# Performance work log

Measured on AMD Instinct MI355X. Metric: run time of the kernel, lower is better.

## Reference

```python
import jax, jax.numpy as jnp
import numpy as np

NVAR, B, C, H, W = 3, 4, 256, 64, 64
C1 = C // 2          # dat channels (nc)
C2 = C - C1
HEADS = 4
HC = C1 // HEADS     # head channels
STRIDE = 4
KS = 4
HK, WK = H // STRIDE, W // STRIDE
NS = HK * WK         # n_sample
RPE_H, RPE_W = 2 * H - 1, 2 * W - 1
NPAIR = 3


def _grid_sample(img, grid):
    # img [B,C,Hi,Wi]; grid [B,Hg,Wg,2] = (x,y) in [-1,1]; bilinear, align_corners=True, zero-pad
    Bn, Cn, Hi, Wi = img.shape
    x = (grid[..., 0] + 1.0) * 0.5 * (Wi - 1)
    y = (grid[..., 1] + 1.0) * 0.5 * (Hi - 1)
    x0 = jnp.floor(x)
    y0 = jnp.floor(y)
    wx = x - x0
    wy = y - y0
    x0i = x0.astype(jnp.int32)
    y0i = y0.astype(jnp.int32)
    imt = img.transpose(0, 2, 3, 1)  # [B,Hi,Wi,C]
    bidx = jnp.arange(Bn)[:, None, None]

    def corner(yi, xi, wgt):
        ok = ((xi >= 0) & (xi < Wi) & (yi >= 0) & (yi < Hi)).astype(img.dtype)
        val = imt[bidx, jnp.clip(yi, 0, Hi - 1), jnp.clip(xi, 0, Wi - 1)]  # [B,Hg,Wg,C]
        return val * (wgt * ok)[..., None]

    out = (corner(y0i, x0i, (1 - wx) * (1 - wy))
           + corner(y0i, x0i + 1, wx * (1 - wy))
           + corner(y0i + 1, x0i, (1 - wx) * wy)
           + corner(y0i + 1, x0i + 1, wx * wy))
    return out.transpose(0, 3, 1, 2)  # [B,C,Hg,Wg]


def _ref_points(hk, wk):
    # normalized sampling-grid reference points, (y,x) order
    ry = (jnp.linspace(0.5, hk - 0.5, hk) / (hk - 1.0)) * 2.0 - 1.0
    rx = (jnp.linspace(0.5, wk - 0.5, wk) / (wk - 1.0)) * 2.0 - 1.0
    return jnp.stack(jnp.meshgrid(ry, rx, indexing='ij'), axis=-1)  # [hk,wk,2]


def _q_grid(h, w):
    gy = (jnp.arange(h, dtype=jnp.float32) / (h - 1.0)) * 2.0 - 1.0
    gx = (jnp.arange(w, dtype=jnp.float32) / (w - 1.0)) * 2.0 - 1.0
    return jnp.stack(jnp.meshgrid(gy, gx, indexing='ij'), axis=-1).reshape(h * w, 2)


def _conv1x1(x, w, b=None):
    y = jnp.einsum('oc,bchw->bohw', w, x)
    return y if b is None else y + b[None, :, None, None]


def _dat_block(q_in, kv_in, pWq, pbq, pWk, pbk, pWv, pbv, pWo, pbo,
               pdw_w, pdw_b, pln_g, pln_b, ppw_w, prpe):
    Bn = q_in.shape[0]
    q = _conv1x1(q_in, pWq, pbq)  # [B,C1,H,W]
    # offset net: depthwise 4x4 stride-4 conv -> channel LN -> GELU -> 1x1 conv to 2
    off = jax.lax.conv_general_dilated(
        q, pdw_w, (STRIDE, STRIDE), 'VALID',
        dimension_numbers=('NCHW', 'OIHW', 'NCHW'),
        feature_group_count=C1) + pdw_b[None, :, None, None]  # [B,C1,HK,WK]
    mu = off.mean(axis=1, keepdims=True)
    var = ((off - mu) ** 2).mean(axis=1, keepdims=True)
    off = (off - mu) * jax.lax.rsqrt(var + 1e-5) * pln_g[None, :, None, None] + pln_b[None, :, None, None]
    off = jax.nn.gelu(off, approximate=False)
    offset = _conv1x1(off, ppw_w).transpose(0, 2, 3, 1)  # [B,HK,WK,2] (dy,dx)
    # offset_range_factor = -1 -> no tanh scaling, clamp pos into [-1,1]
    pos = jnp.clip(offset + _ref_points(HK, WK)[None], -1.0, 1.0)  # [B,HK,WK,2]
    xs = _grid_sample(kv_in, pos[..., ::-1])  # sample kv at deformed points -> [B,C1,HK,WK]
    k = _conv1x1(xs, pWk, pbk).reshape(Bn, HEADS, HC, NS)
    v = _conv1x1(xs, pWv, pbv).reshape(Bn, HEADS, HC, NS)
    qh = q.reshape(Bn, HEADS, HC, H * W)
    attn = jnp.einsum('bhcm,bhcn->bhmn', qh, k) * (HC ** -0.5)  # [B,h,HW,NS]
    # relative position bias sampled from rpe table
    disp = (_q_grid(H, W)[None, :, None, :] - pos.reshape(Bn, 1, NS, 2)) * 0.5  # [B,HW,NS,2]
    rpe_b = jnp.broadcast_to(prpe[None], (Bn, HEADS, RPE_H, RPE_W))
    bias = _grid_sample(rpe_b, disp[..., ::-1])  # [B,h,HW,NS]
    attn = jax.nn.softmax(attn + bias, axis=-1)
    out = jnp.einsum('bhmn,bhcn->bhcm', attn, v).reshape(Bn, C1, H, W)
    return _conv1x1(out, pWo, pbo)


def _forward(xs, params):
    results = []
    num = 0
    for i in range(NVAR):
        res = xs[i]
        for j in range(i):
            attn_out = _dat_block(xs[i][:, :C1], xs[j][:, :C1],
                                  *(p[num] for p in params))
            # torch: res -= -cat(zeros[:,:C2], attn)  => add attn on channels C2:
            res = res.at[:, C2:].add(attn_out)
            num += 1
        results.append(res)
    return jnp.stack(results)  # [NVAR,B,C,H,W]


def setup_inputs() -> dict:
    key = jax.random.key(0)
    ks = jax.random.split(key, 4)
    d = {}
    for n, k in zip(['x0', 'x1', 'x2'], jax.random.split(ks[0], 3)):
        d[n] = jax.random.normal(k, (B, C, H, W), jnp.float32)

    def w(k, shape, s=0.02):
        return jax.random.normal(k, shape, jnp.float32) * s

    kk = jax.random.split(ks[1], 8)
    d['Wq'] = w(kk[0], (NPAIR, C1, C1))
    d['bq'] = jnp.zeros((NPAIR, C1), jnp.float32)
    d['Wk'] = w(kk[1], (NPAIR, C1, C1))
    d['bk'] = jnp.zeros((NPAIR, C1), jnp.float32)
    d['Wv'] = w(kk[2], (NPAIR, C1, C1))
    d['bv'] = jnp.zeros((NPAIR, C1), jnp.float32)
    d['Wo'] = w(kk[3], (NPAIR, C1, C1))
    d['bo'] = jnp.zeros((NPAIR, C1), jnp.float32)
    d['dw_w'] = w(kk[4], (NPAIR, C1, 1, KS, KS), 0.1)
    d['dw_b'] = jnp.zeros((NPAIR, C1), jnp.float32)
    d['ln_g'] = jnp.ones((NPAIR, C1), jnp.float32)
    d['ln_b'] = jnp.zeros((NPAIR, C1), jnp.float32)
    d['pw_w'] = w(kk[5], (NPAIR, 2, C1), 0.1)
    d['rpe'] = w(kk[6], (NPAIR, HEADS, RPE_H, RPE_W), 0.01)
    return d


def reference(x0, x1, x2, Wq, bq, Wk, bk, Wv, bv, Wo, bo,
              dw_w, dw_b, ln_g, ln_b, pw_w, rpe):
    params = (Wq, bq, Wk, bk, Wv, bv, Wo, bo, dw_w, dw_b, ln_g, ln_b, pw_w, rpe)
    out = _forward([x0, x1, x2], params)
    flow = jnp.zeros((NVAR, x0.shape[0]), out.dtype)
    return out, flow
```

## Files before the change

### kernel.cpp

```cpp
#include <hip/hip_runtime.h>
#include <math.h>

#define NVAR 3
#define BB 4
#define CC 256
#define C1 128
#define HEADS 4
#define HH 64
#define WW 64
#define HW 4096
#define RPE_W 127
#define NP 3
#define SCALE 0.17677669529663687f

typedef short bf16x8 __attribute__((ext_vector_type(8)));
typedef float f32x4 __attribute__((ext_vector_type(4)));
typedef __bf16 bf16x2 __attribute__((ext_vector_type(2)));

__device__ __forceinline__ unsigned short f2bf(float f) {
    unsigned int u = __float_as_uint(f);
    u += 0x7fffu + ((u >> 16) & 1u);
    return (unsigned short)(u >> 16);
}
__device__ __forceinline__ float bflo(unsigned u) { return __uint_as_float(u << 16); }
__device__ __forceinline__ float bfhi(unsigned u) { return __uint_as_float(u & 0xffff0000u); }

__device__ __forceinline__ float dot2bf(unsigned a, unsigned b, float c) {
#if __has_builtin(__builtin_amdgcn_fdot2_f32_bf16)
    return __builtin_amdgcn_fdot2_f32_bf16(__builtin_bit_cast(bf16x2, a),
                                           __builtin_bit_cast(bf16x2, b), c, false);
#else
    return c + bflo(a) * bflo(b) + bfhi(a) * bfhi(b);
#endif
}

__global__ __launch_bounds__(256) void prep_copy(const float* __restrict__ rpe,
                                                 const float* __restrict__ Wq,
                                                 const float* __restrict__ Wo,
                                                 const float* __restrict__ Wk,
                                                 const float* __restrict__ Wv,
                                                 const float* __restrict__ x0,
                                                 unsigned short* __restrict__ tabbf,
                                                 unsigned short* __restrict__ wqh,
                                                 unsigned short* __restrict__ woh,
                                                 unsigned short* __restrict__ wkh,
                                                 unsigned short* __restrict__ wvh,
                                                 float* __restrict__ out) {
    int blk = blockIdx.x;
    if (blk >= 24) {
        const long long n4 = (long long)BB * CC * HW / 4;
        long long i = (long long)(blk - 24) * 256 + threadIdx.x;
        const long long stride = 1024LL * 256;
        for (; i < n4 + 12; i += stride) {
            if (i < n4) ((float4*)out)[i] = ((const float4*)x0)[i];
            else out[3LL * BB * CC * HW + (i - n4)] = 0.f;
        }
        return;
    }
    if (blk < 12) {
        const float* src = rpe + (long long)blk * RPE_W * RPE_W;
        unsigned short* dst = tabbf + (long long)blk * 16384;
        for (int idx = threadIdx.x; idx < 16384; idx += 256) {
            int y = idx >> 7, x = idx & 127;
            float v = (y < RPE_W && x < RPE_W) ? src[y * RPE_W + x] : 0.f;
            dst[idx] = f2bf(v);
        }
    } else if (blk < 15) {
        int p = blk - 12;
        for (int i = threadIdx.x; i < 16384; i += 256)
            wqh[p * 16384 + i] = f2bf(Wq[p * 16384 + i]);
    } else if (blk < 18) {
        int p = blk - 15;
        for (int i = threadIdx.x; i < 16384; i += 256)
            woh[p * 16384 + i] = f2bf(Wo[p * 16384 + i]);
    } else if (blk < 21) {
        int p = blk - 18;
        for (int i = threadIdx.x; i < 16384; i += 256)
            wkh[p * 16384 + i] = f2bf(Wk[p * 16384 + i]);
    } else {
        int p = blk - 21;
        for (int i = threadIdx.x; i < 16384; i += 256)
            wvh[p * 16384 + i] = f2bf(Wv[p * 16384 + i]);
    }
}

__global__ __launch_bounds__(256) void conv_q(const float* __restrict__ x1,
                                              const float* __restrict__ x2,
                                              const unsigned short* __restrict__ wqh,
                                              const float* __restrict__ bq,
                                              unsigned short* __restrict__ qbf,
                                              float* __restrict__ out) {
    __shared__ unsigned short qlds[4][16][136];
    int wid = threadIdx.x >> 6, lane = threadIdx.x & 63;
    int g = lane >> 4, lm = lane & 15;
    int gw = blockIdx.x * 4 + wid;
    int mt = gw & 255;
    int pbi = gw >> 8;
    int merged = pbi >> 2;
    int b = pbi & 3;
    const float* X = (merged ? x2 : x1) + (long long)b * CC * HW;
    int m = mt * 16 + lm;
    int qi = merged + 1;
    float* outc = out + (((long long)(qi * 4 + b)) * CC) * HW + m;

    bf16x8 bh[4];
#pragma unroll
    for (int ksl = 0; ksl < 4; ksl++) {
        float v[8];
#pragma unroll
        for (int j = 0; j < 8; j++) {
            int k = ksl * 32 + 8 * g + j;
            v[j] = X[(long long)k * HW + m];
            outc[(long long)k * HW] = v[j];
        }
        union { unsigned u[4]; bf16x8 v; } H;
#pragma unroll
        for (int t = 0; t < 4; t++)
            H.u[t] = (unsigned)f2bf(v[2 * t]) | ((unsigned)f2bf(v[2 * t + 1]) << 16);
        bh[ksl] = H.v;
    }

    f32x4 zero = {0.f, 0.f, 0.f, 0.f};
    unsigned short* ql = &qlds[wid][lm][0];
    int qq = lane >> 4, cg = lane & 15;

    for (int rep = 0; rep <= merged; rep++) {
        int p = merged ? (1 + rep) : 0;
        int pb = p * 4 + b;
        const unsigned short* WH = wqh + p * 16384;
#pragma unroll
        for (int ct2 = 0; ct2 < 4; ct2++) {
            int ct0 = 2 * ct2, ct1 = ct0 + 1;
            f32x4 a0 = zero, a1 = zero;
#pragma unroll
            for (int ksl = 0; ksl < 4; ksl++) {
                bf16x8 Ah0 = *(const bf16x8*)(WH + (ct0 * 16 + lm) * 128 + ksl * 32 + 8 * g);
                bf16x8 Ah1 = *(const bf16x8*)(WH + (ct1 * 16 + lm) * 128 + ksl * 32 + 8 * g);
                a0 = __builtin_amdgcn_mfma_f32_16x16x32_bf16(Ah0, bh[ksl], a0, 0, 0, 0);
                a1 = __builtin_amdgcn_mfma_f32_16x16x32_bf16(Ah1, bh[ksl], a1, 0, 0, 0);
            }
            float q0[4], q1[4];
#pragma unroll
            for (int r = 0; r < 4; r++) {
                q0[r] = a0[r] + bq[p * 128 + ct0 * 16 + 4 * g + r];
                q1[r] = a1[r] + bq[p * 128 + ct1 * 16 + 4 * g + r];
            }
            *(unsigned*)(ql + ct0 * 16 + 4 * g) =
                (unsigned)f2bf(q0[0] * SCALE) | ((unsigned)f2bf(q0[1] * SCALE) << 16);
            *(unsigned*)(ql + ct0 * 16 + 4 * g + 2) =
                (unsigned)f2bf(q0[2] * SCALE) | ((unsigned)f2bf(q0[3] * SCALE) << 16);
            *(unsigned*)(ql + ct1 * 16 + 4 * g) =
                (unsigned)f2bf(q1[0] * SCALE) | ((unsigned)f2bf(q1[1] * SCALE) << 16);
            *(unsigned*)(ql + ct1 * 16 + 4 * g + 2) =
                (unsigned)f2bf(q1[2] * SCALE) | ((unsigned)f2bf(q1[3] * SCALE) << 16);
        }
        unsigned short* Yb = qbf + ((long long)pb * HW + mt * 16) * 128;
#pragma unroll
        for (int i = 0; i < 4; i++) {
            int row = i * 4 + qq;
            uint4 vv = *(const uint4*)&qlds[wid][row][cg * 8];
            *(uint4*)(Yb + row * 128 + cg * 8) = vv;
        }
    }
}

__global__ __launch_bounds__(256) void mid_kernel(const unsigned short* __restrict__ qbf,
                                                  const float* __restrict__ dw_w,
                                                  const float* __restrict__ dw_b,
                                                  const float* __restrict__ ln_g,
                                                  const float* __restrict__ ln_b,
                                                  const float* __restrict__ pw_w,
                                                  const float* __restrict__ x0,
                                                  const float* __restrict__ x1,
                                                  float* __restrict__ posb,
                                                  uint4* __restrict__ prmb,
                                                  unsigned short* __restrict__ xT) {
    __shared__ char sm[40960];
    int blk = blockIdx.x;
    int tid = threadIdx.x;
    if (blk < 192) {
        unsigned short* qs = (unsigned short*)sm;
        float (*dwout)[128] = (float(*)[128])(sm + 32768);
        int pb = blk >> 4, hk = blk & 15;
        int p = pb >> 2;
        int c = tid & 127;
        int wk0 = tid >> 7;
        const float* dwp_g = dw_w + (p * 128 + c) * 16;
        float dwp[16];
#pragma unroll
        for (int j = 0; j < 16; j++) dwp[j] = dwp_g[j] * (1.f / SCALE);
        float acc[8];
#pragma unroll
        for (int o = 0; o < 8; o++) acc[o] = dw_b[p * 128 + c];
        const unsigned short* Q = qbf + ((long long)pb * HW + hk * 256) * 128;
        for (int pass = 0; pass < 2; pass++) {
            __syncthreads();
#pragma unroll
            for (int it = 0; it < 8; it++) {
                int idx = tid + it * 256;
                int mloc = idx >> 4, cg = idx & 15;
                *(uint4*)(qs + mloc * 128 + cg * 8) =
                    *(const uint4*)(Q + (long long)(pass * 128 + mloc) * 128 + cg * 8);
            }
            __syncthreads();
#pragma unroll
            for (int o = 0; o < 8; o++) {
                int wk = wk0 + o * 2;
                float a = acc[o];
#pragma unroll
                for (int kyl = 0; kyl < 2; kyl++)
#pragma unroll
                    for (int kx = 0; kx < 4; kx++)
                        a += bflo((unsigned)qs[(kyl * 64 + wk * 4 + kx) * 128 + c])
                             * dwp[(pass * 2 + kyl) * 4 + kx];
                acc[o] = a;
            }
        }
        __syncthreads();
#pragma unroll
        for (int o = 0; o < 8; o++) dwout[wk0 + o * 2][c] = acc[o];
        __syncthreads();
        int wid = tid >> 6, lane = tid & 63;
        for (int i = 0; i < 4; i++) {
            int wk = wid * 4 + i;
            int s = hk * 16 + wk;
            float a0 = dwout[wk][lane], a1 = dwout[wk][lane + 64];
            float s1 = a0 + a1;
#pragma unroll
            for (int o = 1; o < 64; o <<= 1) s1 += __shfl_xor(s1, o);
            float mu = s1 * (1.f / 128.f);
            float d0 = a0 - mu, d1 = a1 - mu;
            float v2 = d0 * d0 + d1 * d1;
#pragma unroll
            for (int o = 1; o < 64; o <<= 1) v2 += __shfl_xor(v2, o);
            float rs = rsqrtf(v2 * (1.f / 128.f) + 1e-5f);
            int c0 = lane, c1 = lane + 64;
            float y0 = d0 * rs * ln_g[p * 128 + c0] + ln_b[p * 128 + c0];
            float y1 = d1 * rs * ln_g[p * 128 + c1] + ln_b[p * 128 + c1];
            float g0 = 0.5f * y0 * (1.f + erff(y0 * 0.70710678118654752f));
            float g1 = 0.5f * y1 * (1.f + erff(y1 * 0.70710678118654752f));
            float o0 = pw_w[(p * 2 + 0) * 128 + c0] * g0
                     + pw_w[(p * 2 + 0) * 128 + c1] * g1;
            float o1 = pw_w[(p * 2 + 1) * 128 + c0] * g0
                     + pw_w[(p * 2 + 1) * 128 + c1] * g1;
#pragma unroll
            for (int o = 1; o < 64; o <<= 1) o0 += __shfl_xor(o0, o);
#pragma unroll
            for (int o = 1; o < 64; o <<= 1) o1 += __shfl_xor(o1, o);
            if (lane == 0) {
                int wk2 = s & 15;
                float refy = (hk + 0.5f) * (2.f / 15.f) - 1.f;
                float refx = (wk2 + 0.5f) * (2.f / 15.f) - 1.f;
                float py = fminf(fmaxf(o0 + refy, -1.f), 1.f);
                float px = fminf(fmaxf(o1 + refx, -1.f), 1.f);
                int pbn = pb * 256 + s;
                posb[pbn * 2 + 0] = py;
                posb[pbn * 2 + 1] = px;
                float cy = 31.5f * (1.f - py), cx = 31.5f * (1.f - px);
                float yf = floorf(cy), xf = floorf(cx);
                float wy = cy - yf, wx = cx - xf;
                int Y0 = (int)yf, X0 = (int)xf;
                uint4 v;
                v.x = (unsigned)f2bf((1.f - wy) * (1.f - wx))
                    | ((unsigned)f2bf((1.f - wy) * wx) << 16);
                v.y = (unsigned)f2bf(wy * (1.f - wx))
                    | ((unsigned)f2bf(wy * wx) << 16);
                v.z = (unsigned)((Y0 * 128 + X0) * 2);
                v.w = 0;
                prmb[pbn] = v;
            }
        }
    } else {
        float (*ld2)[65] = (float(*)[65])sm;
        int rem = blk - 192;
        int v = rem >> 10;
        int rem1 = rem & 1023;
        int b = rem1 >> 8;
        int rem2 = rem1 & 255;
        int ct = rem2 >> 6;
        int mt = rem2 & 63;
        const float* src = ((v == 0) ? x0 : x1) + (long long)b * CC * HW
                           + (long long)(ct * 32) * HW + mt * 64;
#pragma unroll
        for (int it = 0; it < 2; it++) {
            int c = tid >> 3, x4 = (tid & 7) + it * 8;
            float4 w = *(const float4*)(src + (long long)c * HW + x4 * 4);
            ld2[c][x4 * 4 + 0] = w.x;
            ld2[c][x4 * 4 + 1] = w.y;
            ld2[c][x4 * 4 + 2] = w.z;
            ld2[c][x4 * 4 + 3] = w.w;
        }
        __syncthreads();
        int m = tid >> 2, cg = tid & 3;
        union { unsigned u[4]; } pk;
#pragma unroll
        for (int t = 0; t < 4; t++) {
            unsigned short h0 = f2bf(ld2[cg * 8 + 2 * t][m]);
            unsigned short h1 = f2bf(ld2[cg * 8 + 2 * t + 1][m]);
            pk.u[t] = (unsigned)h0 | ((unsigned)h1 << 16);
        }
        *(uint4*)(xT + (((long long)(v * 4 + b)) * HW + mt * 64 + m) * 128
                  + ct * 32 + cg * 8) = *(uint4*)pk.u;
    }
}

__global__ __launch_bounds__(256) void sample_kv(const unsigned short* __restrict__ xT,
                                                 const float* __restrict__ posb,
                                                 const unsigned short* __restrict__ wkh,
                                                 const unsigned short* __restrict__ wvh,
                                                 const float* __restrict__ bk,
                                                 const float* __restrict__ bv,
                                                 unsigned short* __restrict__ kbf,
                                                 unsigned short* __restrict__ vbf) {
    __shared__ unsigned short xls[32 * 128];
    int blk = blockIdx.x;
    int pb = blk >> 3;
    int nt = blk & 7;
    int p = pb >> 2, b = pb & 3;
    int n0 = nt * 32;
    int tid = threadIdx.x;

    {
        int nl = tid >> 3, co = tid & 7;
        int n = n0 + nl;
        float py = posb[(pb * 256 + n) * 2 + 0];
        float px = posb[(pb * 256 + n) * 2 + 1];
        float yi = (py + 1.f) * 31.5f, xi = (px + 1.f) * 31.5f;
        yi = fminf(fmaxf(yi, 0.f), 63.f);
        xi = fminf(fmaxf(xi, 0.f), 63.f);
        int y0 = min((int)yi, 62);
        int x0i = min((int)xi, 62);
        float wy = yi - (float)y0, wx = xi - (float)x0i;
        float w00 = (1.f - wy) * (1.f - wx), w01 = (1.f - wy) * wx;
        float w10 = wy * (1.f - wx), w11 = wy * wx;
        int vsel = (p == 2) ? 1 : 0;
        const unsigned short* base = xT + ((long long)(vsel * 4 + b)) * HW * 128;
        int m00 = y0 * 64 + x0i;
        char* dst = (char*)xls;
#pragma unroll
        for (int cb = 0; cb < 2; cb++) {
            int c0 = co * 16 + cb * 8;
            bf16x8 a = *(const bf16x8*)(base + (long long)m00 * 128 + c0);
            bf16x8 bb = *(const bf16x8*)(base + (long long)(m00 + 1) * 128 + c0);
            bf16x8 cc = *(const bf16x8*)(base + (long long)(m00 + 64) * 128 + c0);
            bf16x8 dd = *(const bf16x8*)(base + (long long)(m00 + 65) * 128 + c0);
            union { unsigned u[4]; bf16x8 v; } R;
#pragma unroll
            for (int t = 0; t < 4; t++) {
                float r0 = w00 * bflo((unsigned)(unsigned short)a[2 * t])
                         + w01 * bflo((unsigned)(unsigned short)bb[2 * t])
                         + w10 * bflo((unsigned)(unsigned short)cc[2 * t])
                         + w11 * bflo((unsigned)(unsigned short)dd[2 * t]);
                float r1 = w00 * bflo((unsigned)(unsigned short)a[2 * t + 1])
                         + w01 * bflo((unsigned)(unsigned short)bb[2 * t + 1])
                         + w10 * bflo((unsigned)(unsigned short)cc[2 * t + 1])
                         + w11 * bflo((unsigned)(unsigned short)dd[2 * t + 1]);
                R.u[t] = (unsigned)f2bf(r0) | ((unsigned)f2bf(r1) << 16);
            }
            *(bf16x8*)(dst + ((nl * 256 + c0 * 2) ^ ((nl & 7) << 4))) = R.v;
        }
    }
    __syncthreads();

    int wid = tid >> 6, lane = tid & 63;
    int g = lane >> 4, lm = lane & 15;
    int ntile = wid & 1, isv = wid >> 1;
    int nl = ntile * 16 + lm;
    const char* srcl = (const char*)xls;
    bf16x8 xf[4];
#pragma unroll
    for (int ks = 0; ks < 4; ks++)
        xf[ks] = *(const bf16x8*)(srcl + ((nl * 256 + (ks * 32 + 8 * g) * 2)
                                          ^ ((nl & 7) << 4)));
    f32x4 zero = {0.f, 0.f, 0.f, 0.f};
    if (!isv) {
        const unsigned short* WK = wkh + p * 16384;
#pragma unroll
        for (int ct = 0; ct < 8; ct++) {
            f32x4 acc = zero;
#pragma unroll
            for (int ks = 0; ks < 4; ks++) {
                bf16x8 wf = *(const bf16x8*)(WK + (ct * 16 + lm) * 128 + ks * 32 + 8 * g);
                acc = __builtin_amdgcn_mfma_f32_16x16x32_bf16(xf[ks], wf, acc, 0, 0, 0);
            }
            float bias = bk[p * 128 + ct * 16 + lm];
#pragma unroll
            for (int r = 0; r < 4; r++) {
                int n = n0 + ntile * 16 + 4 * g + r;
                kbf[((long long)pb * 256 + n) * 128 + ct * 16 + lm] = f2bf(acc[r] + bias);
            }
        }
    } else {
        const unsigned short* WV = wvh + p * 16384;
#pragma unroll
        for (int ct = 0; ct < 8; ct++) {
            f32x4 acc = zero;
#pragma unroll
            for (int ks = 0; ks < 4; ks++) {
                bf16x8 wf = *(const bf16x8*)(WV + (ct * 16 + lm) * 128 + ks * 32 + 8 * g);
                acc = __builtin_amdgcn_mfma_f32_16x16x32_bf16(wf, xf[ks], acc, 0, 0, 0);
            }
#pragma unroll
            for (int r = 0; r < 4; r++) {
                int c = ct * 16 + 4 * g + r;
                vbf[((long long)pb * 128 + c) * 256 + n0 + ntile * 16 + lm]
                    = f2bf(acc[r] + bv[p * 128 + c]);
            }
        }
    }
}

__global__ __launch_bounds__(256, 4) void attn_mfma(
        const unsigned short* __restrict__ qbf,
        const unsigned short* __restrict__ kbf,
        const unsigned short* __restrict__ vbf,
        const unsigned short* __restrict__ tabbf,
        const uint4* __restrict__ prmb,
        unsigned short* __restrict__ obf) {
    __shared__ unsigned short tab[16384 + 8];
    __shared__ uint4 prm[256];
    int tid = threadIdx.x;
    int wid = tid >> 6, lane = tid & 63;
    int g = lane >> 4, lm = lane & 15;
    int bid = blockIdx.x;
    int my = bid & 63;
    int h = (bid >> 6) & 3;
    int b = (bid >> 8) & 3;
    int p = bid >> 10;
    int pb = p * 4 + b;

    {
        const uint4* ts = (const uint4*)(tabbf + (long long)(p * 4 + h) * 16384);
        uint4* td = (uint4*)tab;
#pragma unroll
        for (int i = 0; i < 8; i++) td[tid + i * 256] = ts[tid + i * 256];
        prm[tid] = prmb[pb * 256 + tid];
    }
    __syncthreads();

    int mx = (wid << 4) + lm;

    bf16x8 qf = *(const bf16x8*)(qbf + ((long long)pb * HW + my * 64 + mx) * 128
                                 + h * 32 + 8 * g);
    const unsigned short* kbase = kbf + ((long long)pb * 256 + lm) * 128
                                  + h * 32 + 8 * g;
    f32x4 zero = {0.f, 0.f, 0.f, 0.f};
    f32x4 acc[16];
    __builtin_amdgcn_s_setprio(1);
#pragma unroll
    for (int ni = 0; ni < 16; ni++) {
        bf16x8 kf = *(const bf16x8*)(kbase + ni * 16 * 128);
        acc[ni] = __builtin_amdgcn_mfma_f32_16x16x32_bf16(kf, qf, zero, 0, 0, 0);
    }
    __builtin_amdgcn_s_setprio(0);

    int laneoff = (my * 128 + mx) * 2;
    const char* tb = (const char*)tab;
#pragma unroll
    for (int ni = 0; ni < 16; ni++) {
#pragma unroll
        for (int r = 0; r < 4; r++) {
            int n = ni * 16 + 4 * g + r;
            uint4 pw = prm[n];
            int va = (int)pw.z + laneoff;
            int va4 = va & ~3;
            int sh = va & 3;
            unsigned r0 = *(const unsigned*)(tb + va4);
            unsigned r1 = *(const unsigned*)(tb + va4 + 4);
            unsigned r2 = *(const unsigned*)(tb + va4 + 256);
            unsigned r3 = *(const unsigned*)(tb + va4 + 260);
            unsigned p0 = __builtin_amdgcn_alignbyte(r1, r0, sh);
            unsigned p1 = __builtin_amdgcn_alignbyte(r3, r2, sh);
            float t = acc[ni][r];
            t = dot2bf(p0, pw.x, t);
            t = dot2bf(p1, pw.y, t);
            acc[ni][r] = t;
        }
    }

    float mxv = -1e30f;
#pragma unroll
    for (int ni = 0; ni < 16; ni++)
        mxv = fmaxf(mxv, fmaxf(fmaxf(acc[ni][0], acc[ni][1]),
                               fmaxf(acc[ni][2], acc[ni][3])));
    mxv = fmaxf(mxv, __shfl_xor(mxv, 16));
    mxv = fmaxf(mxv, __shfl_xor(mxv, 32));
    float sum = 0.f;
    unsigned dwA[16], dwB[16];
#pragma unroll
    for (int ni = 0; ni < 16; ni++) {
        float e0 = __expf(acc[ni][0] - mxv);
        float e1 = __expf(acc[ni][1] - mxv);
        float e2 = __expf(acc[ni][2] - mxv);
        float e3 = __expf(acc[ni][3] - mxv);
        sum += (e0 + e1) + (e2 + e3);
        asm("v_cvt_pk_bf16_f32 %0, %1, %2" : "=v"(dwA[ni]) : "v"(e0), "v"(e1));
        asm("v_cvt_pk_bf16_f32 %0, %1, %2" : "=v"(dwB[ni]) : "v"(e2), "v"(e3));
    }
    sum += __shfl_xor(sum, 16);
    sum += __shfl_xor(sum, 32);

    int src0 = ((g & 1) << 5) + lm;
    int src1 = src0 + 16;
    bool sel = (g >> 1) != 0;
    const unsigned short* vb0 = vbf + ((long long)pb * 128 + h * 32 + lm) * 256
                                + 8 * g;
    f32x4 o0 = zero, o1 = zero;
#pragma unroll
    for (int st = 0; st < 8; st++) {
        unsigned d0a = __shfl(dwA[2 * st], src0), d0b = __shfl(dwA[2 * st + 1], src0);
        unsigned d1a = __shfl(dwB[2 * st], src0), d1b = __shfl(dwB[2 * st + 1], src0);
        unsigned d2a = __shfl(dwA[2 * st], src1), d2b = __shfl(dwA[2 * st + 1], src1);
        unsigned d3a = __shfl(dwB[2 * st], src1), d3b = __shfl(dwB[2 * st + 1], src1);
        union { unsigned u[4]; bf16x8 v; } pf;
        pf.u[0] = sel ? d0b : d0a;
        pf.u[1] = sel ? d1b : d1a;
        pf.u[2] = sel ? d2b : d2a;
        pf.u[3] = sel ? d3b : d3a;
        bf16x8 v0 = *(const bf16x8*)(vb0 + st * 32);
        bf16x8 v1 = *(const bf16x8*)(vb0 + 4096 + st * 32);
        __builtin_amdgcn_s_setprio(1);
        o0 = __builtin_amdgcn_mfma_f32_16x16x32_bf16(v0, pf.v, o0, 0, 0, 0);
        o1 = __builtin_amdgcn_mfma_f32_16x16x32_bf16(v1, pf.v, o1, 0, 0, 0);
        __builtin_amdgcn_s_setprio(0);
    }

    float inv = 1.f / sum;
    __syncthreads();
    {
        unsigned short* rw = tab + wid * 640 + lm * 40;
        *(unsigned*)(rw + g * 4) =
            (unsigned)f2bf(o0[0] * inv) | ((unsigned)f2bf(o0[1] * inv) << 16);
        *(unsigned*)(rw + g * 4 + 2) =
            (unsigned)f2bf(o0[2] * inv) | ((unsigned)f2bf(o0[3] * inv) << 16);
        *(unsigned*)(rw + 16 + g * 4) =
            (unsigned)f2bf(o1[0] * inv) | ((unsigned)f2bf(o1[1] * inv) << 16);
        *(unsigned*)(rw + 16 + g * 4 + 2) =
            (unsigned)f2bf(o1[2] * inv) | ((unsigned)f2bf(o1[3] * inv) << 16);
    }
    int row = lane >> 2, cb = lane & 3;
    uint4 vv = *(const uint4*)(tab + wid * 640 + row * 40 + cb * 8);
    *(uint4*)(obf + ((long long)pb * HW + my * 64 + wid * 16 + row) * 128
              + h * 32 + cb * 8) = vv;
}

__global__ __launch_bounds__(256) void conv_wo(const float* __restrict__ x1,
                                               const float* __restrict__ x2,
                                               const unsigned short* __restrict__ obf,
                                               const unsigned short* __restrict__ woh,
                                               const float* __restrict__ bo,
                                               float* __restrict__ out) {
    int wid = threadIdx.x >> 6, lane = threadIdx.x & 63;
    int g = lane >> 4, lm = lane & 15;
    int gw = blockIdx.x * 4 + wid;
    int mt = gw & 255;
    int b = (gw >> 8) & 3;
    int vs = gw >> 10;
    int m = mt * 16 + lm;
    int np = vs + 1;

    f32x4 acc[8];
#pragma unroll
    for (int ct = 0; ct < 8; ct++) acc[ct] = (f32x4){0.f, 0.f, 0.f, 0.f};

    for (int pi = 0; pi < np; pi++) {
        int p = vs ? (1 + pi) : 0;
        const unsigned short* Om = obf + ((long long)(p * 4 + b) * HW + m) * 128;
        const unsigned short* WH = woh + p * 16384;
#pragma unroll
        for (int ksl = 0; ksl < 4; ksl++) {
            bf16x8 bh = *(const bf16x8*)(Om + ksl * 32 + 8 * g);
#pragma unroll
            for (int ct = 0; ct < 8; ct++) {
                bf16x8 A = *(const bf16x8*)(WH + (ct * 16 + lm) * 128 + ksl * 32 + 8 * g);
                acc[ct] = __builtin_amdgcn_mfma_f32_16x16x32_bf16(A, bh, acc[ct], 0, 0, 0);
            }
        }
    }

    int qi = vs + 1;
    const float* xq = (vs ? x2 : x1) + (long long)b * CC * HW;
#pragma unroll
    for (int ct = 0; ct < 8; ct++)
#pragma unroll
        for (int r = 0; r < 4; r++) {
            int c = ct * 16 + 4 * g + r;
            float bias = vs ? (bo[128 + c] + bo[256 + c]) : bo[c];
            float base = xq[(long long)(128 + c) * HW + m];
            out[(((long long)(qi * 4 + b)) * CC + 128 + c) * HW + m]
                = base + acc[ct][r] + bias;
        }
}

extern "C" void kernel_launch(void* const* d_in, const int* in_sizes, int n_in,
                              void* d_out, int out_size, void* d_ws, size_t ws_size,
                              hipStream_t stream) {
    const float* x0 = (const float*)d_in[0];
    const float* x1 = (const float*)d_in[1];
    const float* x2 = (const float*)d_in[2];
    const float* Wq = (const float*)d_in[3];
    const float* bq = (const float*)d_in[4];
    const float* Wk = (const float*)d_in[5];
    const float* bk = (const float*)d_in[6];
    const float* Wv = (const float*)d_in[7];
    const float* bv = (const float*)d_in[8];
    const float* Wo = (const float*)d_in[9];
    const float* bo = (const float*)d_in[10];
    const float* dw_w = (const float*)d_in[11];
    const float* dw_b = (const float*)d_in[12];
    const float* ln_g = (const float*)d_in[13];
    const float* ln_b = (const float*)d_in[14];
    const float* pw_w = (const float*)d_in[15];
    const float* rpe = (const float*)d_in[16];
    float* out = (float*)d_out;

    float* ws = (float*)d_ws;
    unsigned short* obf = (unsigned short*)ws;
    float* posb = ws + 6291456;
    unsigned short* xT = (unsigned short*)(posb + 6144);
    unsigned short* qbf = xT + 4194304;
    unsigned short* kbf = qbf + 12582912;
    unsigned short* vbf = kbf + 393216;
    unsigned short* tabbf = vbf + 393216;
    uint4* prmb = (uint4*)(tabbf + 196608);
    unsigned short* wqh = (unsigned short*)(prmb + 3072);
    unsigned short* woh = wqh + 49152;
    unsigned short* wkh = woh + 49152;
    unsigned short* wvh = wkh + 49152;

    prep_copy<<<1048, 256, 0, stream>>>(rpe, Wq, Wo, Wk, Wv, x0, tabbf,
                                        wqh, woh, wkh, wvh, out);
    conv_q<<<512, 256, 0, stream>>>(x1, x2, wqh, bq, qbf, out);
    mid_kernel<<<2240, 256, 0, stream>>>(qbf, dw_w, dw_b, ln_g, ln_b, pw_w,
                                         x0, x1, posb, prmb, xT);
    sample_kv<<<96, 256, 0, stream>>>(xT, posb, wkh, wvh, bk, bv, kbf, vbf);
    attn_mfma<<<3072, 256, 0, stream>>>(qbf, kbf, vbf, tabbf, prmb, obf);
    conv_wo<<<512, 256, 0, stream>>>(x1, x2, obf, woh, bo, out);
}
```

Measured before the change: 163.1 us.

## Split attention key dimension across two wave groups with LDS softmax merge

```diff
diff --git a/kernel.cpp b/kernel.cpp
--- a/kernel.cpp
+++ b/kernel.cpp
@@ -410,7 +410,7 @@
     }
 }
 
-__global__ __launch_bounds__(256, 4) void attn_mfma(
+__global__ __launch_bounds__(512, 4) void attn_mfma(
         const unsigned short* __restrict__ qbf,
         const unsigned short* __restrict__ kbf,
         const unsigned short* __restrict__ vbf,
@@ -422,6 +422,8 @@
     int tid = threadIdx.x;
     int wid = tid >> 6, lane = tid & 63;
     int g = lane >> 4, lm = lane & 15;
+    int nh = wid >> 2;
+    int mq = wid & 3;
     int bid = blockIdx.x;
     int my = bid & 63;
     int h = (bid >> 6) & 3;
@@ -433,23 +435,24 @@
         const uint4* ts = (const uint4*)(tabbf + (long long)(p * 4 + h) * 16384);
         uint4* td = (uint4*)tab;
 #pragma unroll
-        for (int i = 0; i < 8; i++) td[tid + i * 256] = ts[tid + i * 256];
-        prm[tid] = prmb[pb * 256 + tid];
+        for (int i = 0; i < 4; i++) td[tid + i * 512] = ts[tid + i * 512];
+        if (tid < 256) prm[tid] = prmb[pb * 256 + tid];
     }
     __syncthreads();
 
-    int mx = (wid << 4) + lm;
+    int mx = (mq << 4) + lm;
+    int nb = nh * 128;
 
     bf16x8 qf = *(const bf16x8*)(qbf + ((long long)pb * HW + my * 64 + mx) * 128
                                  + h * 32 + 8 * g);
     const unsigned short* kbase = kbf + ((long long)pb * 256 + lm) * 128
                                   + h * 32 + 8 * g;
     f32x4 zero = {0.f, 0.f, 0.f, 0.f};
-    f32x4 acc[16];
+    f32x4 acc[8];
     __builtin_amdgcn_s_setprio(1);
 #pragma unroll
-    for (int ni = 0; ni < 16; ni++) {
-        bf16x8 kf = *(const bf16x8*)(kbase + ni * 16 * 128);
+    for (int ni = 0; ni < 8; ni++) {
+        bf16x8 kf = *(const bf16x8*)(kbase + (nb + ni * 16) * 128);
         acc[ni] = __builtin_amdgcn_mfma_f32_16x16x32_bf16(kf, qf, zero, 0, 0, 0);
     }
     __builtin_amdgcn_s_setprio(0);
@@ -457,10 +460,10 @@
     int laneoff = (my * 128 + mx) * 2;
     const char* tb = (const char*)tab;
 #pragma unroll
-    for (int ni = 0; ni < 16; ni++) {
+    for (int ni = 0; ni < 8; ni++) {
 #pragma unroll
         for (int r = 0; r < 4; r++) {
-            int n = ni * 16 + 4 * g + r;
+            int n = nb + ni * 16 + 4 * g + r;
             uint4 pw = prm[n];
             int va = (int)pw.z + laneoff;
             int va4 = va & ~3;
@@ -478,36 +481,46 @@
         }
     }
 
-    float mxv = -1e30f;
-#pragma unroll
-    for (int ni = 0; ni < 16; ni++)
-        mxv = fmaxf(mxv, fmaxf(fmaxf(acc[ni][0], acc[ni][1]),
-                               fmaxf(acc[ni][2], acc[ni][3])));
-    mxv = fmaxf(mxv, __shfl_xor(mxv, 16));
-    mxv = fmaxf(mxv, __shfl_xor(mxv, 32));
-    float sum = 0.f;
-    unsigned dwA[16], dwB[16];
-#pragma unroll
-    for (int ni = 0; ni < 16; ni++) {
-        float e0 = __expf(acc[ni][0] - mxv);
-        float e1 = __expf(acc[ni][1] - mxv);
-        float e2 = __expf(acc[ni][2] - mxv);
-        float e3 = __expf(acc[ni][3] - mxv);
-        sum += (e0 + e1) + (e2 + e3);
+    float mloc = -1e30f;
+#pragma unroll
+    for (int ni = 0; ni < 8; ni++)
+        mloc = fmaxf(mloc, fmaxf(fmaxf(acc[ni][0], acc[ni][1]),
+                                 fmaxf(acc[ni][2], acc[ni][3])));
+    mloc = fmaxf(mloc, __shfl_xor(mloc, 16));
+    mloc = fmaxf(mloc, __shfl_xor(mloc, 32));
+
+    float* mex = (float*)tab;
+    float* sex = (float*)tab + 128;
+    float* oex = (float*)tab + 256;
+    __syncthreads();
+    if (g == 0) mex[nh * 64 + mx] = mloc;
+    __syncthreads();
+    float mglob = fmaxf(mex[mx], mex[64 + mx]);
+
+    float lsum = 0.f;
+    unsigned dwA[8], dwB[8];
+#pragma unroll
+    for (int ni = 0; ni < 8; ni++) {
+        float e0 = __expf(acc[ni][0] - mglob);
+        float e1 = __expf(acc[ni][1] - mglob);
+        float e2 = __expf(acc[ni][2] - mglob);
+        float e3 = __expf(acc[ni][3] - mglob);
+        lsum += (e0 + e1) + (e2 + e3);
         asm("v_cvt_pk_bf16_f32 %0, %1, %2" : "=v"(dwA[ni]) : "v"(e0), "v"(e1));
         asm("v_cvt_pk_bf16_f32 %0, %1, %2" : "=v"(dwB[ni]) : "v"(e2), "v"(e3));
     }
-    sum += __shfl_xor(sum, 16);
-    sum += __shfl_xor(sum, 32);
+    lsum += __shfl_xor(lsum, 16);
+    lsum += __shfl_xor(lsum, 32);
+    if (g == 0) sex[nh * 64 + mx] = lsum;
 
     int src0 = ((g & 1) << 5) + lm;
     int src1 = src0 + 16;
     bool sel = (g >> 1) != 0;
     const unsigned short* vb0 = vbf + ((long long)pb * 128 + h * 32 + lm) * 256
-                                + 8 * g;
+                                + 8 * g + nb;
     f32x4 o0 = zero, o1 = zero;
 #pragma unroll
-    for (int st = 0; st < 8; st++) {
+    for (int st = 0; st < 4; st++) {
         unsigned d0a = __shfl(dwA[2 * st], src0), d0b = __shfl(dwA[2 * st + 1], src0);
         unsigned d1a = __shfl(dwB[2 * st], src0), d1b = __shfl(dwB[2 * st + 1], src0);
         unsigned d2a = __shfl(dwA[2 * st], src1), d2b = __shfl(dwA[2 * st + 1], src1);
@@ -525,10 +538,22 @@
         __builtin_amdgcn_s_setprio(0);
     }
 
-    float inv = 1.f / sum;
+    if (nh == 1) {
+        float* od = oex + (mq * 64 + lane) * 8;
+#pragma unroll
+        for (int r = 0; r < 4; r++) { od[r] = o0[r]; od[4 + r] = o1[r]; }
+    }
     __syncthreads();
+    if (nh == 1) return;
+
+    const float* os = oex + (mq * 64 + lane) * 8;
+#pragma unroll
+    for (int r = 0; r < 4; r++) { o0[r] += os[r]; o1[r] += os[4 + r]; }
+    float inv = 1.f / (sex[mx] + sex[64 + mx]);
+
+    unsigned short* bounce = tab + 6144;
     {
-        unsigned short* rw = tab + wid * 640 + lm * 40;
+        unsigned short* rw = bounce + mq * 640 + lm * 40;
         *(unsigned*)(rw + g * 4) =
             (unsigned)f2bf(o0[0] * inv) | ((unsigned)f2bf(o0[1] * inv) << 16);
         *(unsigned*)(rw + g * 4 + 2) =
@@ -539,8 +564,8 @@
             (unsigned)f2bf(o1[2] * inv) | ((unsigned)f2bf(o1[3] * inv) << 16);
     }
     int row = lane >> 2, cb = lane & 3;
-    uint4 vv = *(const uint4*)(tab + wid * 640 + row * 40 + cb * 8);
-    *(uint4*)(obf + ((long long)pb * HW + my * 64 + wid * 16 + row) * 128
+    uint4 vv = *(const uint4*)(bounce + mq * 640 + row * 40 + cb * 8);
+    *(uint4*)(obf + ((long long)pb * HW + my * 64 + mq * 16 + row) * 128
               + h * 32 + cb * 8) = vv;
 }
 
@@ -634,6 +659,6 @@
     mid_kernel<<<2240, 256, 0, stream>>>(qbf, dw_w, dw_b, ln_g, ln_b, pw_w,
                                          x0, x1, posb, prmb, xT);
     sample_kv<<<96, 256, 0, stream>>>(xT, posb, wkh, wvh, bk, bv, kbf, vbf);
-    attn_mfma<<<3072, 256, 0, stream>>>(qbf, kbf, vbf, tabbf, prmb, obf);
+    attn_mfma<<<3072, 512, 0, stream>>>(qbf, kbf, vbf, tabbf, prmb, obf);
     conv_wo<<<512, 256, 0, stream>>>(x1, x2, obf, woh, bo, out);
 }
```

Result: no change. 161.5 us (-1.0%).
